# Performance work log

Measured on AMD Instinct MI355X. Metric: run time of the kernel, lower is better.

## Reference

```python
import jax, jax.numpy as jnp
import numpy as np
from jax import lax

N_GROUPS = 2
TOPK_GROUPS = 1
TOPK = 4
ROUTE_SCALE = 1.0


def setup_inputs() -> dict:
    key = jax.random.key(0)
    k1, k2 = jax.random.split(key)
    T, D, E = 524288, 256, 64
    x = jax.random.normal(k1, (T, D), dtype=jnp.float32)
    W = jax.random.normal(k2, (E, D), dtype=jnp.float32) * 0.02  # router weight [out, in]
    return {"x": x, "W": W}


def reference(x, W):
    T = x.shape[0]
    E = W.shape[0]
    logits = x @ W.T  # [T, E]
    scores = jax.nn.softmax(logits.astype(jnp.float32), axis=-1)
    original_scores = scores
    # grouped masking (bias is None -> amax group score)
    g = scores.reshape(T, N_GROUPS, E // N_GROUPS)
    group_scores = g.max(axis=-1)  # [T, G]
    _, gidx = lax.top_k(group_scores, TOPK_GROUPS)  # [T, topk_groups]
    keep = jnp.zeros((T, N_GROUPS), dtype=bool).at[jnp.arange(T)[:, None], gidx].set(True)
    masked = jnp.where(keep[:, :, None], g, -jnp.inf).reshape(T, E)
    _, indices = lax.top_k(masked, TOPK)  # [T, topk]
    weights = jnp.take_along_axis(original_scores, indices, axis=1)
    weights = weights * ROUTE_SCALE
    return weights.astype(x.dtype), indices
```

## Files before the change

kernel.cpp:

```cpp
#include <hip/hip_runtime.h>
#include <hip/hip_bf16.h>
#include <stdint.h>


typedef __attribute__((ext_vector_type(8))) short bf16x8;
typedef __attribute__((ext_vector_type(4))) float f32x4;
typedef __attribute__((ext_vector_type(4))) int i32x4;

#define SPLIT_OFF 1024
#define LIST_OFF 102400
#define DELTA 1e-4f

__device__ __forceinline__ f32x4 mf(const i32x4& a, const i32x4& b,
                                    const f32x4& c) {
  return __builtin_amdgcn_mfma_f32_16x16x32_bf16(
      __builtin_bit_cast(bf16x8, a), __builtin_bit_cast(bf16x8, b), c, 0, 0, 0);
}

__device__ __forceinline__ int packhi(unsigned e0, unsigned e1) {
  return (int)__builtin_amdgcn_perm(e1, e0, 0x07060302u);
}

__device__ __forceinline__ void gload16(const void* g, void* l) {
  __builtin_amdgcn_global_load_lds(
      (const __attribute__((address_space(1))) void*)g,
      (__attribute__((address_space(3))) void*)l, 16, 0, 0);
}

__global__ void zero_meta(int* meta) { meta[0] = 0; }

__global__ void split_w(const float* __restrict__ W,
                        unsigned short* __restrict__ ws, int n) {
  int i = blockIdx.x * 256 + threadIdx.x;
  if (i >= n) return;
  float w = W[i];
  unsigned u = __float_as_uint(w);
  unsigned uh = u & 0xFFFF0000u;
  float rf = w - __uint_as_float(uh);
  unsigned short lv[2];
  lv[0] = (unsigned short)(uh >> 16);
  lv[1] = (unsigned short)(__float_as_uint(rf) >> 16);
  int e = i >> 8, k = i & 255;
  int nt = e >> 4, le = e & 15;
  int c = k >> 5, lg = (k >> 3) & 3, kk = k & 7;
  int lane = lg * 16 + le;
#pragma unroll
  for (int v = 0; v < 2; ++v)
    ws[(((c * 8 + v * 4 + nt) * 64) + lane) * 8 + kk] = lv[v];
}

struct XF2 { i32x4 h, m; };

__device__ __forceinline__ XF2 split2(f32x4 a, f32x4 b) {
  float xs[8] = {a[0], a[1], a[2], a[3], b[0], b[1], b[2], b[3]};
  XF2 f;
#pragma unroll
  for (int wd = 0; wd < 4; ++wd) {
    unsigned u0 = __float_as_uint(xs[2 * wd]);
    unsigned u1 = __float_as_uint(xs[2 * wd + 1]);
    f.h[wd] = packhi(u0, u1);
    float r0 = xs[2 * wd] - __uint_as_float(u0 & 0xFFFF0000u);
    float r1 = xs[2 * wd + 1] - __uint_as_float(u1 & 0xFFFF0000u);
    f.m[wd] = packhi(__float_as_uint(r0), __float_as_uint(r1));
  }
  return f;
}

#define GL(dst, ptr, OFF)                                     \
  asm volatile("global_load_dwordx4 %0, %1, off offset:%2"    \
               : "=v"(dst)                                    \
               : "v"(ptr), "n"(OFF))

#define WAITV(NSTR)                                         \
  do {                                                      \
    asm volatile("s_waitcnt vmcnt(" NSTR ")" ::: "memory"); \
    __builtin_amdgcn_sched_barrier(0);                      \
  } while (0)

__global__ __launch_bounds__(256, 2) void gate_kernel(
    const float* __restrict__ x, const unsigned short* __restrict__ wsp,
    float* __restrict__ out, int* __restrict__ meta, int* __restrict__ list,
    int cap, int T) {
  __shared__ i32x4 WL[4096];

  const int t = threadIdx.x;
  const int lane = t & 63;
  const int wid = t >> 6;
  const int le = lane & 15;
  const int lg = lane >> 4;
  const int tokbase = blockIdx.x * 256 + wid * 64;

  const float* xa0 = x + (size_t)(tokbase + le) * 256 + lg * 8;
  const float* xa1 = xa0 + 16 * 256;
  const float* xa2 = xa0 + 32 * 256;
  const float* xa3 = xa0 + 48 * 256;

  f32x4 xbuf[4][8];
  f32x4 acc[4][4];
#pragma unroll
  for (int nt = 0; nt < 4; ++nt)
#pragma unroll
    for (int t4 = 0; t4 < 4; ++t4) acc[nt][t4] = (f32x4)0.0f;

#define STAGE_X(c)                              \
  do {                                          \
    GL(xbuf[(c) & 3][0], xa0, (c) * 128);       \
    GL(xbuf[(c) & 3][1], xa0, (c) * 128 + 16);  \
    GL(xbuf[(c) & 3][2], xa1, (c) * 128);       \
    GL(xbuf[(c) & 3][3], xa1, (c) * 128 + 16);  \
    GL(xbuf[(c) & 3][4], xa2, (c) * 128);       \
    GL(xbuf[(c) & 3][5], xa2, (c) * 128 + 16);  \
    GL(xbuf[(c) & 3][6], xa3, (c) * 128);       \
    GL(xbuf[(c) & 3][7], xa3, (c) * 128 + 16);  \
  } while (0)

#define ITER(c, NSTR)                                                   \
  {                                                                     \
    if ((c) + 3 < 8) STAGE_X((c) + 3);                                  \
    i32x4 wr[8];                                                        \
    _Pragma("unroll") for (int q = 0; q < 8; ++q)                       \
        wr[q] = WL[(((c) * 8 + q) << 6) + lane];                        \
    WAITV(NSTR);                                                        \
    _Pragma("unroll") for (int t4 = 0; t4 < 4; ++t4) {                  \
      XF2 b = split2(xbuf[(c) & 3][2 * t4], xbuf[(c) & 3][2 * t4 + 1]); \
      _Pragma("unroll") for (int nt = 0; nt < 4; ++nt) {                \
        acc[nt][t4] = mf(wr[nt], b.h, acc[nt][t4]);                     \
        acc[nt][t4] = mf(wr[nt], b.m, acc[nt][t4]);                     \
        acc[nt][t4] = mf(wr[4 + nt], b.h, acc[nt][t4]);                 \
        acc[nt][t4] = mf(wr[4 + nt], b.m, acc[nt][t4]);                 \
      }                                                                 \
    }                                                                   \
  }

  {
    const char* wsrc = (const char*)wsp + t * 16;
    char* wdst = (char*)WL + t * 16;
#pragma unroll
    for (int i = 0; i < 16; ++i) gload16(wsrc + i * 4096, wdst + i * 4096);
  }
  STAGE_X(0);
  STAGE_X(1);
  STAGE_X(2);
  WAITV("24");
  __builtin_amdgcn_s_barrier();

  ITER(0, "24");
  ITER(1, "24");
  ITER(2, "24");
  ITER(3, "24");
  ITER(4, "24");
  ITER(5, "16");
  ITER(6, "8");
  ITER(7, "0");

#pragma unroll
  for (int tt = 0; tt < 4; ++tt) {
    float l[16];
#pragma unroll
    for (int nt = 0; nt < 4; ++nt)
#pragma unroll
      for (int j = 0; j < 4; ++j) l[nt * 4 + j] = acc[nt][tt][j];

    float g0 = l[0], g1 = l[8];
#pragma unroll
    for (int j = 1; j < 8; ++j) {
      g0 = fmaxf(g0, l[j]);
      g1 = fmaxf(g1, l[8 + j]);
    }
    g0 = fmaxf(g0, __shfl_xor(g0, 16));
    g0 = fmaxf(g0, __shfl_xor(g0, 32));
    g1 = fmaxf(g1, __shfl_xor(g1, 16));
    g1 = fmaxf(g1, __shfl_xor(g1, 32));
    const int g = (g1 > g0) ? 1 : 0;
    const float m = fmaxf(g0, g1);

    float sum = 0.f;
#pragma unroll
    for (int k = 0; k < 16; ++k) sum += __expf(l[k] - m);
    sum += __shfl_xor(sum, 16);
    sum += __shfl_xor(sum, 32);
    const float inv = 1.0f / sum;

    float c[8];
    int ce[8];
#pragma unroll
    for (int j2 = 0; j2 < 8; ++j2) {
      c[j2] = l[g * 8 + j2];
      ce[j2] = (2 * g + (j2 >> 2)) * 16 + 4 * lg + (j2 & 3);
    }

    float v5[5];
    int e5[5];
#pragma unroll
    for (int it = 0; it < 5; ++it) {
      float bv = c[0];
      int be = ce[0];
#pragma unroll
      for (int j2 = 1; j2 < 8; ++j2) {
        bool gt = c[j2] > bv;
        bv = gt ? c[j2] : bv;
        be = gt ? ce[j2] : be;
      }
#pragma unroll
      for (int st = 0; st < 2; ++st) {
        int msk = 16 << st;
        float ov = __shfl_xor(bv, msk);
        int oe = __shfl_xor(be, msk);
        bool tk = (ov > bv) || (ov == bv && oe < be);
        bv = tk ? ov : bv;
        be = tk ? oe : be;
      }
      v5[it] = bv;
      e5[it] = be;
#pragma unroll
      for (int j2 = 0; j2 < 8; ++j2)
        c[j2] = (ce[j2] == be) ? -3.0e38f : c[j2];
    }

    float ming = fabsf(g0 - g1);
#pragma unroll
    for (int it = 0; it < 4; ++it) ming = fminf(ming, v5[it] - v5[it + 1]);

    if (lg == 0) {
      size_t trow = (size_t)tokbase + tt * 16 + le;
      *(float4*)&out[trow * 4] =
          make_float4(__expf(v5[0] - m) * inv, __expf(v5[1] - m) * inv,
                      __expf(v5[2] - m) * inv, __expf(v5[3] - m) * inv);
      *(float4*)&out[(size_t)T * 4 + trow * 4] = make_float4(
          (float)e5[0], (float)e5[1], (float)e5[2], (float)e5[3]);
      if (ming < DELTA) {
        int p = atomicAdd(meta, 1);
        if (p < cap) list[p] = (int)trow;
      }
    }
  }
}

__global__ __launch_bounds__(64) void fix_kernel(
    const float* __restrict__ x, const float* __restrict__ W,
    float* __restrict__ out, const int* __restrict__ meta,
    const int* __restrict__ list, int cap, int T) {
  const int e = threadIdx.x;
  int cnt = meta[0];
  cnt = cnt < cap ? cnt : cap;
  for (int i = blockIdx.x; i < cnt; i += gridDim.x) {
    const int tok = list[i];
    const float* xr = x + (size_t)tok * 256;
    const float* wr = W + (size_t)e * 256;
    float acc = 0.f;
#pragma unroll 8
    for (int d = 0; d < 256; d += 4) {
      float4 xv = *(const float4*)(xr + d);
      float4 wv = *(const float4*)(wr + d);
      acc = fmaf(xv.x, wv.x, acc);
      acc = fmaf(xv.y, wv.y, acc);
      acc = fmaf(xv.z, wv.z, acc);
      acc = fmaf(xv.w, wv.w, acc);
    }
    float gm = acc;
#pragma unroll
    for (int st = 0; st < 5; ++st) gm = fmaxf(gm, __shfl_xor(gm, 1 << st));
    float om = __shfl_xor(gm, 32);
    float g0 = (e < 32) ? gm : om;
    float g1 = (e < 32) ? om : gm;
    const int g = (g1 > g0) ? 1 : 0;
    const float m = fmaxf(g0, g1);
    float sum = __expf(acc - m);
#pragma unroll
    for (int st = 0; st < 6; ++st) sum += __shfl_xor(sum, 1 << st);
    const float inv = 1.0f / sum;

    float cand = ((e >> 5) == g) ? acc : -3.0e38f;
    float w4[4], i4[4];
#pragma unroll
    for (int it = 0; it < 4; ++it) {
      float bv = cand;
      int be = e;
#pragma unroll
      for (int st = 0; st < 6; ++st) {
        int msk = 1 << st;
        float ov = __shfl_xor(bv, msk);
        int oe = __shfl_xor(be, msk);
        bool tk = (ov > bv) || (ov == bv && oe < be);
        bv = tk ? ov : bv;
        be = tk ? oe : be;
      }
      w4[it] = __expf(bv - m) * inv;
      i4[it] = (float)be;
      if (e == be) cand = -3.0e38f;
    }
    if (e == 0) {
      *(float4*)&out[(size_t)tok * 4] = make_float4(w4[0], w4[1], w4[2], w4[3]);
      *(float4*)&out[(size_t)T * 4 + (size_t)tok * 4] =
          make_float4(i4[0], i4[1], i4[2], i4[3]);
    }
  }
}

extern "C" void kernel_launch(void* const* d_in, const int* in_sizes, int n_in,
                              void* d_out, int out_size, void* d_ws,
                              size_t ws_size, hipStream_t stream) {
  const float* x = (const float*)d_in[0];
  const float* W = (const float*)d_in[1];
  float* out = (float*)d_out;
  int T = in_sizes[0] / 256;
  int nW = in_sizes[1];
  int* meta = (int*)d_ws;
  unsigned short* wsp = (unsigned short*)((char*)d_ws + SPLIT_OFF);
  int* list = (int*)((char*)d_ws + LIST_OFF);
  int cap = (ws_size > LIST_OFF + 4) ? (int)((ws_size - LIST_OFF) / 4) : 0;
  hipLaunchKernelGGL(zero_meta, dim3(1), dim3(1), 0, stream, meta);
  hipLaunchKernelGGL(split_w, dim3((nW + 255) / 256), dim3(256), 0, stream, W,
                     wsp, nW);
  hipLaunchKernelGGL(gate_kernel, dim3(T / 256), dim3(256), 0, stream, x, wsp,
                     out, meta, list, cap, T);
  hipLaunchKernelGGL(fix_kernel, dim3(2048), dim3(64), 0, stream, x, W, out,
                     meta, list, cap, T);
}
```

Baseline: 145.7 us.

## Halve per-wave token tile, double waves per block, fold meta zeroing into split

Each wave now handles 32 tokens instead of 64. Blocks grow to 512 threads (8 waves) with launch bounds raised to allow 4 blocks per CU. This shrinks the x staging buffers and accumulators per wave and pipelines x loads two chunks ahead instead of three. The W fragments are now read from LDS per MFMA group rather than all at once. The separate zero_meta launch is folded into split_w to remove one kernel launch. The tradeoff is less reuse of each W LDS read per token and shallower memory prefetch, in exchange for more resident waves to hide latency.

```diff
diff --git a/kernel.cpp b/kernel.cpp
--- a/kernel.cpp
+++ b/kernel.cpp
@@ -27,11 +27,11 @@
       (__attribute__((address_space(3))) void*)l, 16, 0, 0);
 }
 
-__global__ void zero_meta(int* meta) { meta[0] = 0; }
-
 __global__ void split_w(const float* __restrict__ W,
-                        unsigned short* __restrict__ ws, int n) {
+                        unsigned short* __restrict__ ws, int n,
+                        int* __restrict__ meta) {
   int i = blockIdx.x * 256 + threadIdx.x;
+  if (i == 0) meta[0] = 0;
   if (i >= n) return;
   float w = W[i];
   unsigned u = __float_as_uint(w);
@@ -77,7 +77,7 @@
     __builtin_amdgcn_sched_barrier(0);                      \
   } while (0)
 
-__global__ __launch_bounds__(256, 2) void gate_kernel(
+__global__ __launch_bounds__(512, 4) void gate_kernel(
     const float* __restrict__ x, const unsigned short* __restrict__ wsp,
     float* __restrict__ out, int* __restrict__ meta, int* __restrict__ list,
     int cap, int T) {
@@ -88,73 +88,68 @@
   const int wid = t >> 6;
   const int le = lane & 15;
   const int lg = lane >> 4;
-  const int tokbase = blockIdx.x * 256 + wid * 64;
+  const int tokbase = blockIdx.x * 256 + wid * 32;
 
   const float* xa0 = x + (size_t)(tokbase + le) * 256 + lg * 8;
   const float* xa1 = xa0 + 16 * 256;
-  const float* xa2 = xa0 + 32 * 256;
-  const float* xa3 = xa0 + 48 * 256;
-
-  f32x4 xbuf[4][8];
-  f32x4 acc[4][4];
+
+  f32x4 xbuf[2][4];
+  f32x4 acc[4][2];
 #pragma unroll
   for (int nt = 0; nt < 4; ++nt)
 #pragma unroll
-    for (int t4 = 0; t4 < 4; ++t4) acc[nt][t4] = (f32x4)0.0f;
+    for (int t2 = 0; t2 < 2; ++t2) acc[nt][t2] = (f32x4)0.0f;
 
 #define STAGE_X(c)                              \
   do {                                          \
-    GL(xbuf[(c) & 3][0], xa0, (c) * 128);       \
-    GL(xbuf[(c) & 3][1], xa0, (c) * 128 + 16);  \
-    GL(xbuf[(c) & 3][2], xa1, (c) * 128);       \
-    GL(xbuf[(c) & 3][3], xa1, (c) * 128 + 16);  \
-    GL(xbuf[(c) & 3][4], xa2, (c) * 128);       \
-    GL(xbuf[(c) & 3][5], xa2, (c) * 128 + 16);  \
-    GL(xbuf[(c) & 3][6], xa3, (c) * 128);       \
-    GL(xbuf[(c) & 3][7], xa3, (c) * 128 + 16);  \
+    GL(xbuf[(c) & 1][0], xa0, (c) * 128);       \
+    GL(xbuf[(c) & 1][1], xa0, (c) * 128 + 16);  \
+    GL(xbuf[(c) & 1][2], xa1, (c) * 128);       \
+    GL(xbuf[(c) & 1][3], xa1, (c) * 128 + 16);  \
   } while (0)
 
-#define ITER(c, NSTR)                                                   \
-  {                                                                     \
-    if ((c) + 3 < 8) STAGE_X((c) + 3);                                  \
-    i32x4 wr[8];                                                        \
-    _Pragma("unroll") for (int q = 0; q < 8; ++q)                       \
-        wr[q] = WL[(((c) * 8 + q) << 6) + lane];                        \
-    WAITV(NSTR);                                                        \
-    _Pragma("unroll") for (int t4 = 0; t4 < 4; ++t4) {                  \
-      XF2 b = split2(xbuf[(c) & 3][2 * t4], xbuf[(c) & 3][2 * t4 + 1]); \
-      _Pragma("unroll") for (int nt = 0; nt < 4; ++nt) {                \
-        acc[nt][t4] = mf(wr[nt], b.h, acc[nt][t4]);                     \
-        acc[nt][t4] = mf(wr[nt], b.m, acc[nt][t4]);                     \
-        acc[nt][t4] = mf(wr[4 + nt], b.h, acc[nt][t4]);                 \
-        acc[nt][t4] = mf(wr[4 + nt], b.m, acc[nt][t4]);                 \
-      }                                                                 \
-    }                                                                   \
+#define ITER(c, NSTR)                                               \
+  {                                                                 \
+    WAITV(NSTR);                                                    \
+    XF2 b0 = split2(xbuf[(c) & 1][0], xbuf[(c) & 1][1]);            \
+    XF2 b1 = split2(xbuf[(c) & 1][2], xbuf[(c) & 1][3]);            \
+    if ((c) + 2 < 8) STAGE_X((c) + 2);                              \
+    _Pragma("unroll") for (int nt = 0; nt < 4; ++nt) {              \
+      i32x4 ah = WL[(((c) * 8 + nt) << 6) + lane];                  \
+      i32x4 am = WL[(((c) * 8 + 4 + nt) << 6) + lane];              \
+      acc[nt][0] = mf(ah, b0.h, acc[nt][0]);                        \
+      acc[nt][0] = mf(ah, b0.m, acc[nt][0]);                        \
+      acc[nt][0] = mf(am, b0.h, acc[nt][0]);                        \
+      acc[nt][0] = mf(am, b0.m, acc[nt][0]);                        \
+      acc[nt][1] = mf(ah, b1.h, acc[nt][1]);                        \
+      acc[nt][1] = mf(ah, b1.m, acc[nt][1]);                        \
+      acc[nt][1] = mf(am, b1.h, acc[nt][1]);                        \
+      acc[nt][1] = mf(am, b1.m, acc[nt][1]);                        \
+    }                                                               \
   }
 
   {
     const char* wsrc = (const char*)wsp + t * 16;
     char* wdst = (char*)WL + t * 16;
 #pragma unroll
-    for (int i = 0; i < 16; ++i) gload16(wsrc + i * 4096, wdst + i * 4096);
+    for (int i = 0; i < 8; ++i) gload16(wsrc + i * 8192, wdst + i * 8192);
   }
   STAGE_X(0);
   STAGE_X(1);
-  STAGE_X(2);
-  WAITV("24");
+  WAITV("8");
   __builtin_amdgcn_s_barrier();
 
-  ITER(0, "24");
-  ITER(1, "24");
-  ITER(2, "24");
-  ITER(3, "24");
-  ITER(4, "24");
-  ITER(5, "16");
-  ITER(6, "8");
+  ITER(0, "4");
+  ITER(1, "4");
+  ITER(2, "4");
+  ITER(3, "4");
+  ITER(4, "4");
+  ITER(5, "4");
+  ITER(6, "4");
   ITER(7, "0");
 
 #pragma unroll
-  for (int tt = 0; tt < 4; ++tt) {
+  for (int tt = 0; tt < 2; ++tt) {
     float l[16];
 #pragma unroll
     for (int nt = 0; nt < 4; ++nt)
@@ -309,10 +304,9 @@
   unsigned short* wsp = (unsigned short*)((char*)d_ws + SPLIT_OFF);
   int* list = (int*)((char*)d_ws + LIST_OFF);
   int cap = (ws_size > LIST_OFF + 4) ? (int)((ws_size - LIST_OFF) / 4) : 0;
-  hipLaunchKernelGGL(zero_meta, dim3(1), dim3(1), 0, stream, meta);
   hipLaunchKernelGGL(split_w, dim3((nW + 255) / 256), dim3(256), 0, stream, W,
-                     wsp, nW);
-  hipLaunchKernelGGL(gate_kernel, dim3(T / 256), dim3(256), 0, stream, x, wsp,
+                     wsp, nW, meta);
+  hipLaunchKernelGGL(gate_kernel, dim3(T / 256), dim3(512), 0, stream, x, wsp,
                      out, meta, list, cap, T);
   hipLaunchKernelGGL(fix_kernel, dim3(2048), dim3(64), 0, stream, x, W, out,
                      meta, list, cap, T);
```

After: 142.1 us. -2.5%, faster.
